# Kernel optimization log

Measured on AMD Instinct MI355X. Metric: run time of the kernel, lower is better.

The kernel has to match this reference:

```python
import jax, jax.numpy as jnp
import numpy as np

IN_DIM = 2048
HIDDEN = 5120
OUT_DIM = 1024
T = IN_DIM + HIDDEN + OUT_DIM  # total_units = 8192
NPROP = 8
N_PAIRS = T * (T - 1) // 2  # unique symmetric pair weights


def setup_inputs() -> dict:
    key = jax.random.key(0)
    k1, k2, k3 = jax.random.split(key, 3)
    return {
        "inputs": jax.random.normal(k1, (IN_DIM,), dtype=jnp.float32),
        "w_flat": jax.random.normal(k2, (N_PAIRS,), dtype=jnp.float32) * 0.01,
        "b": jax.random.normal(k3, (T,), dtype=jnp.float32) * 0.01,
    }


def _sym_matrix(w_flat):
    # Scatter the flat pair weights into the strict upper triangle, then
    # symmetrize. Diagonal stays zero: a node never attends to itself
    # (neighbor_nodes excludes states[node] in the original).
    iu, ju = jnp.triu_indices(T, k=1)
    M = jnp.zeros((T, T), dtype=w_flat.dtype).at[iu, ju].set(w_flat)
    return M + M.T


def reference(inputs, w_flat, b):
    M = _sym_matrix(w_flat)  # [T, T] symmetric, zero diagonal
    states = jnp.zeros((T,), dtype=inputs.dtype).at[:IN_DIM].set(inputs)

    def step(s, _):
        # new_state[n] = act(sum_{m != n} w_pair(n, m) * s[m] + b[n])
        s_new = jnp.tanh(M @ s + b)
        return s_new, None

    states, _ = jax.lax.scan(step, states, None, length=NPROP)
    return states[-OUT_DIM:]
```

## Files before the change

### kernel.cpp

```cpp
#include <hip/hip_runtime.h>
#include <hip/hip_fp16.h>


constexpr int T     = 8192;
constexpr int IN    = 2048;
constexpr int OUT   = 1024;
constexpr int NPROP = 8;

constexpr int TILE   = 128;
constexpr int NT     = T / TILE;
constexpr int NTILES = NT * (NT + 1) / 2;

__device__ __forceinline__ unsigned triidx(unsigned r, unsigned j) {
    return r * (unsigned)(T - 1) - ((r * (r - 1u)) >> 1) + j - r - 1u;
}

__device__ __forceinline__ int crow(int r) {
    int q = r >> 3, rem = r & 7;
    return r * T - 8 * (4 * q * (q - 1) + q * (rem + 1));
}
constexpr size_t W16_ALLOC = 33587200;

__host__ __device__ __forceinline__ unsigned rowstart(int b) {
    return (unsigned)(b * NT) - (unsigned)((b * (b - 1)) >> 1);
}

__device__ __forceinline__ void tile_decode(unsigned p, int& bi, int& bj) {
    const float A = (float)(2 * NT + 1);
    bi = (int)((A - sqrtf(A * A - 8.0f * (float)p)) * 0.5f);
    if (bi < 0) bi = 0;
    while (rowstart(bi + 1) <= p) ++bi;
    while (rowstart(bi) > p) --bi;
    bj = bi + (int)(p - rowstart(bi));
}

__device__ __forceinline__ uint4 pack8(const float* v) {
    uint4 pk;
    ushort* us = (ushort*)&pk;
    #pragma unroll
    for (int d = 0; d < 8; ++d) us[d] = __half_as_ushort(__float2half_rn(v[d]));
    return pk;
}

__global__ __launch_bounds__(256) void conv_kernel(const float* __restrict__ w,
                                                   __half* __restrict__ w16) {
    unsigned bid = blockIdx.x;
    int sweep = (int)(bid & 7u);
    int bi, bj; tile_decode(bid >> 3, bi, bj);
    int i0 = bi * TILE, j0 = bj * TILE;
    int t = threadIdx.x;
    int r  = i0 + sweep * 16 + (t >> 4);
    int jb = j0 + (t & 15) * 8;

    if (bi != bj || jb > r) {
        const float* src = w + triidx((unsigned)r, (unsigned)jb);
        float v[8];
        #pragma unroll
        for (int d = 0; d < 8; ++d) v[d] = src[d];
        *(uint4*)(w16 + (crow(r) + jb)) = pack8(v);
    } else if (jb + 7 > r) {
        #pragma unroll
        for (int d = 0; d < 8; ++d) {
            int j = jb + d;
            if (j > r)
                w16[crow(r) + j] =
                    __float2half_rn(w[triidx((unsigned)r, (unsigned)j)]);
        }
    }
}

__global__ __launch_bounds__(256) void init_kernel(const float* __restrict__ in,
                                                   float* __restrict__ s,
                                                   float* __restrict__ y) {
    int n = blockIdx.x * 256 + threadIdx.x;
    if (n < T) { s[n] = (n < IN) ? in[n] : 0.0f; y[n] = 0.0f; }
}

__global__ __launch_bounds__(256) void sym_kernel(const __half* __restrict__ w16,
                                                  const float* __restrict__ s,
                                                  float* __restrict__ y, int mode) {
    __shared__ float sIl[TILE], sJl[TILE];
    __shared__ float colpart[4][TILE];

    int bi, bj; tile_decode(blockIdx.x, bi, bj);
    if (mode == 2 && bj < (T - OUT) / TILE) return;
    bool doRow = (mode == 1) ? (bj < IN / TILE) : true;

    int i0 = bi * TILE, j0 = bj * TILE;
    int t = threadIdx.x;
    if (t < TILE) sIl[t] = s[i0 + t];
    else          sJl[t - TILE] = s[j0 + (t - TILE)];
    __syncthreads();

    int l = t & 63, wv = t >> 6;
    int g = l & 15, ro = l >> 4;
    int cbase = j0 + g * 8;

    float sjv[8];
    #pragma unroll
    for (int d = 0; d < 8; ++d) sjv[d] = sJl[g * 8 + d];
    float colacc[8] = {0.f, 0.f, 0.f, 0.f, 0.f, 0.f, 0.f, 0.f};

    #pragma unroll
    for (int k = 0; k < 8; ++k) {
        int rr = wv * 32 + k * 4 + ro;
        int r  = i0 + rr;
        uint4 wq = *(const uint4*)(w16 + (crow(r) + cbase));
        const __half2* h2 = (const __half2*)&wq;
        float2 f0 = __half22float2(h2[0]);
        float2 f1 = __half22float2(h2[1]);
        float2 f2 = __half22float2(h2[2]);
        float2 f3 = __half22float2(h2[3]);
        float wf[8] = {f0.x, f0.y, f1.x, f1.y, f2.x, f2.y, f3.x, f3.y};

        float si = sIl[rr];
        float rp = 0.0f;
        #pragma unroll
        for (int d = 0; d < 8; ++d) {
            float we = (cbase + d > r) ? wf[d] : 0.0f;
            colacc[d] = fmaf(we, si, colacc[d]);
            rp        = fmaf(we, sjv[d], rp);
        }
        if (doRow) {
            rp += __shfl_xor(rp, 1, 64);
            rp += __shfl_xor(rp, 2, 64);
            rp += __shfl_xor(rp, 4, 64);
            rp += __shfl_xor(rp, 8, 64);
            if (g == 0) atomicAdd(&y[r], rp);
        }
    }

    #pragma unroll
    for (int d = 0; d < 8; ++d) {
        colacc[d] += __shfl_xor(colacc[d], 16, 64);
        colacc[d] += __shfl_xor(colacc[d], 32, 64);
    }
    if (l < 16) {
        #pragma unroll
        for (int d = 0; d < 8; ++d) colpart[wv][g * 8 + d] = colacc[d];
    }
    __syncthreads();
    if (t < TILE) {
        float c = colpart[0][t] + colpart[1][t] + colpart[2][t] + colpart[3][t];
        atomicAdd(&y[j0 + t], c);
    }
}

__global__ __launch_bounds__(256) void act_kernel(const float* __restrict__ b,
                                                  float* __restrict__ s,
                                                  float* __restrict__ y) {
    int n = blockIdx.x * 256 + threadIdx.x;
    if (n < T) { s[n] = tanhf(y[n] + b[n]); y[n] = 0.0f; }
}

__global__ __launch_bounds__(256) void actout_kernel(const float* __restrict__ b,
                                                     const float* __restrict__ y,
                                                     float* __restrict__ o) {
    int n = blockIdx.x * 256 + threadIdx.x;
    if (n < OUT) o[n] = tanhf(y[T - OUT + n] + b[T - OUT + n]);
}

extern "C" void kernel_launch(void* const* d_in, const int* in_sizes, int n_in,
                              void* d_out, int out_size, void* d_ws, size_t ws_size,
                              hipStream_t stream) {
    const float* in = (const float*)d_in[0];
    const float* w  = (const float*)d_in[1];
    const float* b  = (const float*)d_in[2];
    float* out = (float*)d_out;

    __half* w16 = (__half*)d_ws;
    float*  s   = (float*)((char*)d_ws + W16_ALLOC * sizeof(__half));
    float*  y   = s + T;

    conv_kernel<<<NTILES * 8, 256, 0, stream>>>(w, w16);
    init_kernel<<<T / 256, 256, 0, stream>>>(in, s, y);

    sym_kernel<<<rowstart(IN / TILE), 256, 0, stream>>>(w16, s, y, 1);
    act_kernel<<<T / 256, 256, 0, stream>>>(b, s, y);
    for (int it = 1; it < NPROP - 1; ++it) {
        sym_kernel<<<NTILES, 256, 0, stream>>>(w16, s, y, 0);
        act_kernel<<<T / 256, 256, 0, stream>>>(b, s, y);
    }
    sym_kernel<<<NTILES, 256, 0, stream>>>(w16, s, y, 2);
    actout_kernel<<<OUT / 256, 256, 0, stream>>>(b, y, out);
}
```

Baseline: 183.5 us.

## Fuse fp32-to-fp16 weight conversion into first two propagation passes

Removes the standalone conversion kernel and instead converts weights on the fly inside the first two sym_kernel passes. Each pass reads fp32 weights for its assigned tiles, uses them directly, and writes the fp16 copy for later passes. This avoids one full pass over the weight matrix. The final pass also skips row reductions for tiles that do not contribute to the output rows. The cost is uneven work and extra branching in the converting passes.

```diff
diff --git a/kernel.cpp b/kernel.cpp
--- a/kernel.cpp
+++ b/kernel.cpp
@@ -42,33 +42,6 @@
     return pk;
 }
 
-__global__ __launch_bounds__(256) void conv_kernel(const float* __restrict__ w,
-                                                   __half* __restrict__ w16) {
-    unsigned bid = blockIdx.x;
-    int sweep = (int)(bid & 7u);
-    int bi, bj; tile_decode(bid >> 3, bi, bj);
-    int i0 = bi * TILE, j0 = bj * TILE;
-    int t = threadIdx.x;
-    int r  = i0 + sweep * 16 + (t >> 4);
-    int jb = j0 + (t & 15) * 8;
-
-    if (bi != bj || jb > r) {
-        const float* src = w + triidx((unsigned)r, (unsigned)jb);
-        float v[8];
-        #pragma unroll
-        for (int d = 0; d < 8; ++d) v[d] = src[d];
-        *(uint4*)(w16 + (crow(r) + jb)) = pack8(v);
-    } else if (jb + 7 > r) {
-        #pragma unroll
-        for (int d = 0; d < 8; ++d) {
-            int j = jb + d;
-            if (j > r)
-                w16[crow(r) + j] =
-                    __float2half_rn(w[triidx((unsigned)r, (unsigned)j)]);
-        }
-    }
-}
-
 __global__ __launch_bounds__(256) void init_kernel(const float* __restrict__ in,
                                                    float* __restrict__ s,
                                                    float* __restrict__ y) {
@@ -76,7 +49,8 @@
     if (n < T) { s[n] = (n < IN) ? in[n] : 0.0f; y[n] = 0.0f; }
 }
 
-__global__ __launch_bounds__(256) void sym_kernel(const __half* __restrict__ w16,
+__global__ __launch_bounds__(256) void sym_kernel(const float* __restrict__ w32,
+                                                  __half* __restrict__ w16,
                                                   const float* __restrict__ s,
                                                   float* __restrict__ y, int mode) {
     __shared__ float sIl[TILE], sJl[TILE];
@@ -84,7 +58,10 @@
 
     int bi, bj; tile_decode(blockIdx.x, bi, bj);
     if (mode == 2 && bj < (T - OUT) / TILE) return;
-    bool doRow = (mode == 1) ? (bj < IN / TILE) : true;
+    bool doRow = (mode == 0 || mode == 3) ? true
+               : (mode == 1) ? (bj < IN / TILE)
+                             : (bi >= (T - OUT) / TILE);
+    bool f32path = (mode == 1) || (mode == 3 && bi >= IN / TILE);
 
     int i0 = bi * TILE, j0 = bj * TILE;
     int t = threadIdx.x;
@@ -105,13 +82,33 @@
     for (int k = 0; k < 8; ++k) {
         int rr = wv * 32 + k * 4 + ro;
         int r  = i0 + rr;
-        uint4 wq = *(const uint4*)(w16 + (crow(r) + cbase));
-        const __half2* h2 = (const __half2*)&wq;
-        float2 f0 = __half22float2(h2[0]);
-        float2 f1 = __half22float2(h2[1]);
-        float2 f2 = __half22float2(h2[2]);
-        float2 f3 = __half22float2(h2[3]);
-        float wf[8] = {f0.x, f0.y, f1.x, f1.y, f2.x, f2.y, f3.x, f3.y};
+        float wf[8];
+
+        if (!f32path) {
+            uint4 wq = *(const uint4*)(w16 + (crow(r) + cbase));
+            const __half2* h2 = (const __half2*)&wq;
+            float2 f0 = __half22float2(h2[0]);
+            float2 f1 = __half22float2(h2[1]);
+            float2 f2 = __half22float2(h2[2]);
+            float2 f3 = __half22float2(h2[3]);
+            wf[0]=f0.x; wf[1]=f0.y; wf[2]=f1.x; wf[3]=f1.y;
+            wf[4]=f2.x; wf[5]=f2.y; wf[6]=f3.x; wf[7]=f3.y;
+        } else if (bi != bj || cbase > r) {
+            __builtin_memcpy(wf, w32 + triidx((unsigned)r, (unsigned)cbase), 32);
+            *(uint4*)(w16 + (crow(r) + cbase)) = pack8(wf);
+        } else if (r < cbase + 7) {
+            #pragma unroll
+            for (int d = 0; d < 8; ++d) {
+                int j = cbase + d;
+                if (j > r) {
+                    wf[d] = w32[triidx((unsigned)r, (unsigned)j)];
+                    w16[crow(r) + j] = __float2half_rn(wf[d]);
+                } else wf[d] = 0.0f;
+            }
+        } else {
+            #pragma unroll
+            for (int d = 0; d < 8; ++d) wf[d] = 0.0f;
+        }
 
         float si = sIl[rr];
         float rp = 0.0f;
@@ -172,15 +169,16 @@
     float*  s   = (float*)((char*)d_ws + W16_ALLOC * sizeof(__half));
     float*  y   = s + T;
 
-    conv_kernel<<<NTILES * 8, 256, 0, stream>>>(w, w16);
     init_kernel<<<T / 256, 256, 0, stream>>>(in, s, y);
 
-    sym_kernel<<<rowstart(IN / TILE), 256, 0, stream>>>(w16, s, y, 1);
+    sym_kernel<<<rowstart(IN / TILE), 256, 0, stream>>>(w, w16, s, y, 1);
     act_kernel<<<T / 256, 256, 0, stream>>>(b, s, y);
-    for (int it = 1; it < NPROP - 1; ++it) {
-        sym_kernel<<<NTILES, 256, 0, stream>>>(w16, s, y, 0);
+    sym_kernel<<<NTILES, 256, 0, stream>>>(w, w16, s, y, 3);
+    act_kernel<<<T / 256, 256, 0, stream>>>(b, s, y);
+    for (int it = 2; it < NPROP - 1; ++it) {
+        sym_kernel<<<NTILES, 256, 0, stream>>>(w, w16, s, y, 0);
         act_kernel<<<T / 256, 256, 0, stream>>>(b, s, y);
     }
-    sym_kernel<<<NTILES, 256, 0, stream>>>(w16, s, y, 2);
+    sym_kernel<<<NTILES, 256, 0, stream>>>(w, w16, s, y, 2);
     actout_kernel<<<OUT / 256, 256, 0, stream>>>(b, y, out);
 }
```

Result: slower. 226.0 us (+23.1%).
